# Optimization experiments

Measured on AMD Instinct MI355X. Metric: run time of the kernel, lower is better.

## Reference

```python
import jax, jax.numpy as jnp
import numpy as np

B = 64          # number of scenes/graphs
OBJS = 2048     # objects per scene
N = B * OBJS    # total objects
D = 256         # representation_dim
K = 2           # num_channels


def setup_inputs() -> dict:
    key = jax.random.key(0)
    k1, k2, k3 = jax.random.split(key, 3)
    x_aggregation = jax.random.normal(k1, (N, D), dtype=jnp.float32)
    num_objs = jnp.full((B,), OBJS, dtype=jnp.int32)
    # glorot for att_shared [1, D]: fan_in + fan_out = 1 + D
    std_shared = float(np.sqrt(6.0 / (1 + D)))
    att_shared = jax.random.uniform(k2, (1, D), dtype=jnp.float32,
                                    minval=-std_shared, maxval=std_shared)
    # glorot for att_scale [K, 1]
    std_scale = float(np.sqrt(6.0 / (K + 1)))
    att_scale = jax.random.uniform(k3, (K, 1), dtype=jnp.float32,
                                   minval=-std_scale, maxval=std_scale)
    channel_bias = jnp.zeros((K, D), dtype=jnp.float32)
    return {"x_aggregation": x_aggregation, "num_objs": num_objs,
            "att_shared": att_shared, "att_scale": att_scale,
            "channel_bias": channel_bias}


def reference(x_aggregation, num_objs, att_shared, att_scale, channel_bias):
    batch_idx = jnp.repeat(jnp.arange(B), num_objs, total_repeat_length=N)  # [N]
    # scatter_mean: per-scene context features [B, D]
    seg_sum = jax.ops.segment_sum(x_aggregation, batch_idx, num_segments=B)
    counts = jnp.maximum(num_objs, 1).astype(x_aggregation.dtype)
    ctx = seg_sum / counts[:, None]
    attn_in = jax.nn.leaky_relu(x_aggregation + ctx[batch_idx], negative_slope=0.2)  # [N, D]
    # per-channel logits: ((attn_in + bias[k]) . att_shared) * scale[k]
    base = attn_in @ att_shared[0]                 # [N]
    bias_term = channel_bias @ att_shared[0]       # [K]
    logits = (base[:, None] + bias_term[None, :]) * att_scale[:, 0][None, :]  # [N, K]
    # per-channel segment softmax over objects within each scene
    m = jax.ops.segment_max(logits, batch_idx, num_segments=B)   # [B, K]
    z = jnp.exp(logits - m[batch_idx])
    s = jax.ops.segment_sum(z, batch_idx, num_segments=B)        # [B, K]
    attn_weights = z / s[batch_idx]                              # [N, K]
    # attention-weighted pooling per channel -> [B, D, K]
    weighted = x_aggregation[:, :, None] * attn_weights[:, None, :]  # [N, D, K]
    scene_features = jax.ops.segment_sum(weighted, batch_idx, num_segments=B)
    return scene_features, attn_weights
```

## Files before the change

kernel.cpp:

```cpp
#include <hip/hip_runtime.h>

#define B    64
#define OBJS 2048
#define NTOT (B * OBJS)
#define D    256
#define K    2
#define S1   16
#define CH   (OBJS / S1)
#define RPW  (CH / 4)

#define WS_P1  0
#define WS_UP  (1024 * 256)
#define WS_ZP  (WS_UP + 1024 * 512)
#define WS_E   (WS_ZP + 1024 * 8)
#define WS_CNT (WS_E + NTOT * 2)

static __device__ __forceinline__ float lrelu02(float v) {
    return v > 0.0f ? v : 0.2f * v;
}

__global__ __launch_bounds__(256, 4) void fused_all(
        const float* __restrict__ x,
        const int* __restrict__ num_objs,
        const float* __restrict__ att_scale,
        const float* __restrict__ att_shared,
        const float* __restrict__ channel_bias,
        float* __restrict__ ws,
        float* __restrict__ out) {
    __shared__ float pl[4 * 576];
    __shared__ float esm[4 * 16];
    __shared__ float sctx[D];
    __shared__ float sbt[2];
    __shared__ int   sfin;

    int blk = blockIdx.x;
    int b = blk >> 4;
    int t = threadIdx.x;
    int w = t >> 6, l = t & 63;
    int r = l & 7, sl = l >> 3;
    int row0 = blk * CH + w * RPW;
    int* cntA = (int*)(ws + WS_CNT);
    int* cntF = cntA + B;

    {
        float4 acc = make_float4(0.f, 0.f, 0.f, 0.f);
        const float* px = x + (size_t)row0 * D + 4 * l;
#pragma unroll 8
        for (int j = 0; j < RPW; ++j) {
            float4 v = *(const float4*)(px + (size_t)j * D);
            acc.x += v.x; acc.y += v.y; acc.z += v.z; acc.w += v.w;
        }
        *(float4*)(pl + w * D + 4 * l) = acc;
        __syncthreads();
        if (t < 64) {
            float4 a = ((const float4*)(pl        ))[t];
            float4 e = ((const float4*)(pl +     D))[t];
            float4 f = ((const float4*)(pl + 2 * D))[t];
            float4 g = ((const float4*)(pl + 3 * D))[t];
            float4 s4 = make_float4(a.x + e.x + f.x + g.x, a.y + e.y + f.y + g.y,
                                    a.z + e.z + f.z + g.z, a.w + e.w + f.w + g.w);
            *(float4*)(ws + WS_P1 + blk * D + 4 * t) = s4;
        }
        __syncthreads();
        if (t == 0) {
            __threadfence();
            atomicAdd(&cntA[b], 1);
            while (__hip_atomic_load(&cntA[b], __ATOMIC_RELAXED,
                                     __HIP_MEMORY_SCOPE_AGENT) < S1)
                __builtin_amdgcn_s_sleep(2);
            __threadfence();
        }
        __syncthreads();
    }

    {
        int cnt = num_objs[b]; if (cnt < 1) cnt = 1;
        float inv = 1.0f / (float)cnt;
        float sum = 0.f;
#pragma unroll
        for (int c = 0; c < S1; ++c) sum += ws[WS_P1 + (b * S1 + c) * D + t];
        sctx[t] = sum * inv;
    }
    if (t < 64) {
        float4 a = ((const float4*)att_shared)[t];
#pragma unroll
        for (int k = 0; k < K; ++k) {
            float4 cb = ((const float4*)(channel_bias + k * D))[t];
            float v = a.x * cb.x + a.y * cb.y + a.z * cb.z + a.w * cb.w;
#pragma unroll
            for (int m = 32; m > 0; m >>= 1) v += __shfl_xor(v, m);
            if (t == 0) sbt[k] = v;
        }
    }
    __syncthreads();

    float4 a4   = ((const float4*)att_shared)[l];
    float4 ctx4 = *(const float4*)(sctx + 4 * l);
    float bt0 = sbt[0], bt1 = sbt[1];
    float s0 = att_scale[0], s1 = att_scale[1];

    float4 acc0 = make_float4(0.f, 0.f, 0.f, 0.f);
    float4 acc1 = make_float4(0.f, 0.f, 0.f, 0.f);
    float z0 = 0.f, z1 = 0.f;
    float e0c = 0.f, e1c = 0.f;
    float* pw = pl  + w * 576;
    float* ew = esm + w * 16;
    const float* px = x + (size_t)row0 * D + 4 * l;

#pragma unroll
    for (int g = 0; g < 4; ++g) {
        float4 v0 = *(const float4*)(px + (size_t)(g * 8 + 0) * D);
        float4 v1 = *(const float4*)(px + (size_t)(g * 8 + 1) * D);
        float4 v2 = *(const float4*)(px + (size_t)(g * 8 + 2) * D);
        float4 v3 = *(const float4*)(px + (size_t)(g * 8 + 3) * D);
        float4 v4 = *(const float4*)(px + (size_t)(g * 8 + 4) * D);
        float4 v5 = *(const float4*)(px + (size_t)(g * 8 + 5) * D);
        float4 v6 = *(const float4*)(px + (size_t)(g * 8 + 6) * D);
        float4 v7 = *(const float4*)(px + (size_t)(g * 8 + 7) * D);

#define PDOT(V) (lrelu02((V).x + ctx4.x) * a4.x + lrelu02((V).y + ctx4.y) * a4.y \
               + lrelu02((V).z + ctx4.z) * a4.z + lrelu02((V).w + ctx4.w) * a4.w)
        pw[l * 9 + 0] = PDOT(v0); pw[l * 9 + 1] = PDOT(v1);
        pw[l * 9 + 2] = PDOT(v2); pw[l * 9 + 3] = PDOT(v3);
        pw[l * 9 + 4] = PDOT(v4); pw[l * 9 + 5] = PDOT(v5);
        pw[l * 9 + 6] = PDOT(v6); pw[l * 9 + 7] = PDOT(v7);
#undef PDOT
        float tr = 0.f;
#pragma unroll
        for (int q = 0; q < 8; ++q) tr += pw[(sl * 8 + q) * 9 + r];
        tr += __shfl_xor(tr, 8);
        tr += __shfl_xor(tr, 16);
        tr += __shfl_xor(tr, 32);

        float e0 = __expf((tr + bt0) * s0);
        float e1 = __expf((tr + bt1) * s1);
        if (((l >> 3) & 3) == g) { e0c = e0; e1c = e1; }
        if (l < 8) { ew[2 * l] = e0; ew[2 * l + 1] = e1; }
        float4 E0 = *(const float4*)(ew + 0);
        float4 E1 = *(const float4*)(ew + 4);
        float4 E2 = *(const float4*)(ew + 8);
        float4 E3 = *(const float4*)(ew + 12);
        z0 += E0.x + E0.z + E1.x + E1.z + E2.x + E2.z + E3.x + E3.z;
        z1 += E0.y + E0.w + E1.y + E1.w + E2.y + E2.w + E3.y + E3.w;

#define ACC(V, EA, EB) { acc0.x += (V).x * (EA); acc0.y += (V).y * (EA);      \
                         acc0.z += (V).z * (EA); acc0.w += (V).w * (EA);      \
                         acc1.x += (V).x * (EB); acc1.y += (V).y * (EB);      \
                         acc1.z += (V).z * (EB); acc1.w += (V).w * (EB); }
        ACC(v0, E0.x, E0.y) ACC(v1, E0.z, E0.w)
        ACC(v2, E1.x, E1.y) ACC(v3, E1.z, E1.w)
        ACC(v4, E2.x, E2.y) ACC(v5, E2.z, E2.w)
        ACC(v6, E3.x, E3.y) ACC(v7, E3.z, E3.w)
#undef ACC
    }

    if (l < 32) ((float2*)(ws + WS_E))[row0 + l] = make_float2(e0c, e1c);
    if (l == 0) {
        ws[WS_ZP + blk * 8 + w * 2 + 0] = z0;
        ws[WS_ZP + blk * 8 + w * 2 + 1] = z1;
    }
    __syncthreads();
    {
        int base = w * (D * K) + l * 8;
        pl[base + 0] = acc0.x; pl[base + 1] = acc1.x;
        pl[base + 2] = acc0.y; pl[base + 3] = acc1.y;
        pl[base + 4] = acc0.z; pl[base + 5] = acc1.z;
        pl[base + 6] = acc0.w; pl[base + 7] = acc1.w;
    }
    __syncthreads();
    if (t < 128) {
        float4 a = ((const float4*)(pl       ))[t];
        float4 e = ((const float4*)(pl +  512))[t];
        float4 f = ((const float4*)(pl + 1024))[t];
        float4 g = ((const float4*)(pl + 1536))[t];
        float4 s4 = make_float4(a.x + e.x + f.x + g.x, a.y + e.y + f.y + g.y,
                                a.z + e.z + f.z + g.z, a.w + e.w + f.w + g.w);
        *(float4*)(ws + WS_UP + (size_t)blk * (D * K) + 4 * t) = s4;
    }

    __syncthreads();
    if (t == 0) {
        __threadfence();
        int old = atomicAdd(&cntF[b], 1);
        sfin = (old == S1 - 1) ? 1 : 0;
        if (sfin) __threadfence();
    }
    __syncthreads();
    if (!sfin) return;

    if (w < 2) {
        float v = ws[WS_ZP + (b * S1 + (l >> 2)) * 8 + (l & 3) * 2 + w];
#pragma unroll
        for (int m = 32; m > 0; m >>= 1) v += __shfl_xor(v, m);
        if (l == 0) sbt[w] = v;
    }
    __syncthreads();
    float zf0 = sbt[0], zf1 = sbt[1];
    float iz0 = 1.0f / zf0, iz1 = 1.0f / zf1;

#pragma unroll
    for (int j = t; j < D * K; j += 256) {
        float ssum = 0.f;
#pragma unroll
        for (int c = 0; c < S1; ++c) ssum += ws[WS_UP + (b * S1 + c) * (D * K) + j];
        out[b * (D * K) + j] = ssum * ((j & 1) ? iz1 : iz0);
    }
    const float4* E = (const float4*)(ws + WS_E);
    float4* W = (float4*)(out + B * D * K);
#pragma unroll
    for (int i = t; i < OBJS / 2; i += 256) {
        float4 e4 = E[b * (OBJS / 2) + i];
        W[b * (OBJS / 2) + i] = make_float4(e4.x * iz0, e4.y * iz1, e4.z * iz0, e4.w * iz1);
    }
}

__global__ __launch_bounds__(256) void k1_partial(const float* __restrict__ x,
                                                  float* __restrict__ ws) {
    __shared__ float red[4 * D];
    int blk = blockIdx.x;
    int w = threadIdx.x >> 6, l = threadIdx.x & 63;
    int row0 = blk * CH + w * RPW;

    float4 acc = make_float4(0.f, 0.f, 0.f, 0.f);
    const float* px = x + (size_t)row0 * D + 4 * l;
#pragma unroll 8
    for (int j = 0; j < RPW; ++j) {
        float4 v = *(const float4*)(px + (size_t)j * D);
        acc.x += v.x; acc.y += v.y; acc.z += v.z; acc.w += v.w;
    }
    *(float4*)(red + w * D + 4 * l) = acc;
    __syncthreads();
    int t = threadIdx.x;
    if (t < 64) {
        float4 a = ((const float4*)(red        ))[t];
        float4 e = ((const float4*)(red +     D))[t];
        float4 f = ((const float4*)(red + 2 * D))[t];
        float4 g = ((const float4*)(red + 3 * D))[t];
        float4 s = make_float4(a.x + e.x + f.x + g.x, a.y + e.y + f.y + g.y,
                               a.z + e.z + f.z + g.z, a.w + e.w + f.w + g.w);
        *(float4*)(ws + WS_P1 + blk * D + 4 * t) = s;
    }
}

__global__ __launch_bounds__(256) void k2_main(const float* __restrict__ x,
                                               const int* __restrict__ num_objs,
                                               const float* __restrict__ att_scale,
                                               const float* __restrict__ att_shared,
                                               const float* __restrict__ channel_bias,
                                               float* __restrict__ ws) {
    __shared__ float pl[4 * 576];
    __shared__ float esm[4 * 16];
    __shared__ float sctx[D];
    __shared__ float sbt[2];

    int blk = blockIdx.x;
    int b = blk >> 4;
    int t = threadIdx.x;
    int w = t >> 6, l = t & 63;
    int r = l & 7, s = l >> 3;
    int row0 = blk * CH + w * RPW;

    {
        int cnt = num_objs[b]; if (cnt < 1) cnt = 1;
        float inv = 1.0f / (float)cnt;
        float sum = 0.f;
#pragma unroll
        for (int c = 0; c < S1; ++c) sum += ws[WS_P1 + (b * S1 + c) * D + t];
        sctx[t] = sum * inv;
    }
    if (t < 64) {
        float4 a = ((const float4*)att_shared)[t];
#pragma unroll
        for (int k = 0; k < K; ++k) {
            float4 cb = ((const float4*)(channel_bias + k * D))[t];
            float v = a.x * cb.x + a.y * cb.y + a.z * cb.z + a.w * cb.w;
#pragma unroll
            for (int m = 32; m > 0; m >>= 1) v += __shfl_xor(v, m);
            if (t == 0) sbt[k] = v;
        }
    }
    __syncthreads();

    float4 a4   = ((const float4*)att_shared)[l];
    float4 ctx4 = *(const float4*)(sctx + 4 * l);
    float bt0 = sbt[0], bt1 = sbt[1];
    float s0 = att_scale[0], s1 = att_scale[1];

    float4 acc0 = make_float4(0.f, 0.f, 0.f, 0.f);
    float4 acc1 = make_float4(0.f, 0.f, 0.f, 0.f);
    float z0 = 0.f, z1 = 0.f;
    float e0c = 0.f, e1c = 0.f;
    float* pw = pl  + w * 576;
    float* ew = esm + w * 16;
    const float* px = x + (size_t)row0 * D + 4 * l;

#pragma unroll
    for (int g = 0; g < 4; ++g) {
        float4 v0 = *(const float4*)(px + (size_t)(g * 8 + 0) * D);
        float4 v1 = *(const float4*)(px + (size_t)(g * 8 + 1) * D);
        float4 v2 = *(const float4*)(px + (size_t)(g * 8 + 2) * D);
        float4 v3 = *(const float4*)(px + (size_t)(g * 8 + 3) * D);
        float4 v4 = *(const float4*)(px + (size_t)(g * 8 + 4) * D);
        float4 v5 = *(const float4*)(px + (size_t)(g * 8 + 5) * D);
        float4 v6 = *(const float4*)(px + (size_t)(g * 8 + 6) * D);
        float4 v7 = *(const float4*)(px + (size_t)(g * 8 + 7) * D);

#define PDOT(V) (lrelu02((V).x + ctx4.x) * a4.x + lrelu02((V).y + ctx4.y) * a4.y \
               + lrelu02((V).z + ctx4.z) * a4.z + lrelu02((V).w + ctx4.w) * a4.w)
        pw[l * 9 + 0] = PDOT(v0); pw[l * 9 + 1] = PDOT(v1);
        pw[l * 9 + 2] = PDOT(v2); pw[l * 9 + 3] = PDOT(v3);
        pw[l * 9 + 4] = PDOT(v4); pw[l * 9 + 5] = PDOT(v5);
        pw[l * 9 + 6] = PDOT(v6); pw[l * 9 + 7] = PDOT(v7);
#undef PDOT
        float tr = 0.f;
#pragma unroll
        for (int q = 0; q < 8; ++q) tr += pw[(s * 8 + q) * 9 + r];
        tr += __shfl_xor(tr, 8);
        tr += __shfl_xor(tr, 16);
        tr += __shfl_xor(tr, 32);

        float e0 = __expf((tr + bt0) * s0);
        float e1 = __expf((tr + bt1) * s1);
        if (((l >> 3) & 3) == g) { e0c = e0; e1c = e1; }
        if (l < 8) { ew[2 * l] = e0; ew[2 * l + 1] = e1; }
        float4 E0 = *(const float4*)(ew + 0);
        float4 E1 = *(const float4*)(ew + 4);
        float4 E2 = *(const float4*)(ew + 8);
        float4 E3 = *(const float4*)(ew + 12);
        z0 += E0.x + E0.z + E1.x + E1.z + E2.x + E2.z + E3.x + E3.z;
        z1 += E0.y + E0.w + E1.y + E1.w + E2.y + E2.w + E3.y + E3.w;

#define ACC(V, EA, EB) { acc0.x += (V).x * (EA); acc0.y += (V).y * (EA);      \
                         acc0.z += (V).z * (EA); acc0.w += (V).w * (EA);      \
                         acc1.x += (V).x * (EB); acc1.y += (V).y * (EB);      \
                         acc1.z += (V).z * (EB); acc1.w += (V).w * (EB); }
        ACC(v0, E0.x, E0.y) ACC(v1, E0.z, E0.w)
        ACC(v2, E1.x, E1.y) ACC(v3, E1.z, E1.w)
        ACC(v4, E2.x, E2.y) ACC(v5, E2.z, E2.w)
        ACC(v6, E3.x, E3.y) ACC(v7, E3.z, E3.w)
#undef ACC
    }

    if (l < 32) ((float2*)(ws + WS_E))[row0 + l] = make_float2(e0c, e1c);
    if (l == 0) {
        ws[WS_ZP + blk * 8 + w * 2 + 0] = z0;
        ws[WS_ZP + blk * 8 + w * 2 + 1] = z1;
    }
    __syncthreads();
    {
        int base = w * (D * K) + l * 8;
        pl[base + 0] = acc0.x; pl[base + 1] = acc1.x;
        pl[base + 2] = acc0.y; pl[base + 3] = acc1.y;
        pl[base + 4] = acc0.z; pl[base + 5] = acc1.z;
        pl[base + 6] = acc0.w; pl[base + 7] = acc1.w;
    }
    __syncthreads();
    if (t < 128) {
        float4 a = ((const float4*)(pl       ))[t];
        float4 e = ((const float4*)(pl +  512))[t];
        float4 f = ((const float4*)(pl + 1024))[t];
        float4 g = ((const float4*)(pl + 1536))[t];
        float4 s4 = make_float4(a.x + e.x + f.x + g.x, a.y + e.y + f.y + g.y,
                                a.z + e.z + f.z + g.z, a.w + e.w + f.w + g.w);
        *(float4*)(ws + WS_UP + (size_t)blk * (D * K) + 4 * t) = s4;
    }
}

__global__ __launch_bounds__(256) void k3_final(const float* __restrict__ ws,
                                                float* __restrict__ out) {
    __shared__ float zsh[2];
    int b = blockIdx.x;
    int t = threadIdx.x;
    int w = t >> 6, l = t & 63;

    if (w < 2) {
        float v = ws[WS_ZP + (b * S1 + (l >> 2)) * 8 + (l & 3) * 2 + w];
#pragma unroll
        for (int m = 32; m > 0; m >>= 1) v += __shfl_xor(v, m);
        if (l == 0) zsh[w] = v;
    }
    __syncthreads();
    float z0 = zsh[0], z1 = zsh[1];
    float iz0 = 1.0f / z0, iz1 = 1.0f / z1;

#pragma unroll
    for (int j = t; j < D * K; j += 256) {
        float s = 0.f;
#pragma unroll
        for (int c = 0; c < S1; ++c) s += ws[WS_UP + (b * S1 + c) * (D * K) + j];
        out[b * (D * K) + j] = s * ((j & 1) ? iz1 : iz0);
    }
    const float4* E = (const float4*)(ws + WS_E);
    float4* W = (float4*)(out + B * D * K);
#pragma unroll
    for (int i = t; i < OBJS / 2; i += 256) {
        float4 e = E[b * (OBJS / 2) + i];
        W[b * (OBJS / 2) + i] = make_float4(e.x * iz0, e.y * iz1, e.z * iz0, e.w * iz1);
    }
}

extern "C" void kernel_launch(void* const* d_in, const int* in_sizes, int n_in,
                              void* d_out, int out_size, void* d_ws, size_t ws_size,
                              hipStream_t stream) {
    const float* x            = (const float*)d_in[0];
    const int*   num_objs     = (const int*)d_in[1];
    const float* att_shared   = (const float*)d_in[2];
    const float* att_scale    = (const float*)d_in[3];
    const float* channel_bias = (const float*)d_in[4];
    float* ws  = (float*)d_ws;
    float* out = (float*)d_out;

    static int coop_ok = -1;
    if (coop_ok < 0) {
        int nb = 0;
        hipError_t e = hipOccupancyMaxActiveBlocksPerMultiprocessor(
                &nb, fused_all, 256, 0);
        coop_ok = (e == hipSuccess && nb >= 4) ? 1 : 0;
    }

    if (coop_ok) {
        hipMemsetAsync((char*)d_ws + sizeof(float) * (size_t)WS_CNT, 0,
                       2 * B * sizeof(int), stream);
        void* args[] = {(void*)&x, (void*)&num_objs, (void*)&att_scale,
                        (void*)&att_shared, (void*)&channel_bias,
                        (void*)&ws, (void*)&out};
        hipError_t e = hipLaunchCooperativeKernel((void*)fused_all,
                                                  dim3(B * S1), dim3(256),
                                                  args, 0, stream);
        if (e == hipSuccess) return;
        coop_ok = 0;
    }

    k1_partial<<<B * S1, 256, 0, stream>>>(x, ws);
    k2_main<<<B * S1, 256, 0, stream>>>(x, num_objs, att_scale, att_shared,
                                        channel_bias, ws);
    k3_final<<<B, 256, 0, stream>>>(ws, out);
}
```

Measured before the change: 222.3 us.

## Cache x rows in registers and LDS to avoid second global read

The cooperative fused kernel now runs 256 blocks (4 per scene, one per CU) instead of 1024. Each wave keeps its first 80 rows in registers (kp) and the next 32 rows in 128 KB of dynamic LDS while computing the context sum. The softmax/pooling pass then reuses those buffered rows and reloads only the last 16 rows from global memory, which removes most of the second read of x. In exchange, occupancy drops to one large block per CU with very high register pressure, which risks spills and leaves little latency hiding.

Result: no change. 221.1 us (-0.5%).

```diff
diff --git a/kernel.cpp b/kernel.cpp
--- a/kernel.cpp
+++ b/kernel.cpp
@@ -5,6 +5,12 @@
 #define NTOT (B * OBJS)
 #define D    256
 #define K    2
+
+#define NBLK 256
+#define BPS  4
+#define CHF  (OBJS / BPS)
+#define RPWF (CHF / 4)
+
 #define S1   16
 #define CH   (OBJS / S1)
 #define RPW  (CH / 4)
@@ -19,7 +25,7 @@
     return v > 0.0f ? v : 0.2f * v;
 }
 
-__global__ __launch_bounds__(256, 4) void fused_all(
+__global__ __launch_bounds__(256, 1) void fused_all(
         const float* __restrict__ x,
         const int* __restrict__ num_objs,
         const float* __restrict__ att_scale,
@@ -27,6 +33,7 @@
         const float* __restrict__ channel_bias,
         float* __restrict__ ws,
         float* __restrict__ out) {
+    extern __shared__ float4 xbuf4[];
     __shared__ float pl[4 * 576];
     __shared__ float esm[4 * 16];
     __shared__ float sctx[D];
@@ -34,44 +41,277 @@
     __shared__ int   sfin;
 
     int blk = blockIdx.x;
+    int b = blk / BPS;
+    int t = threadIdx.x;
+    int w = t >> 6, l = t & 63;
+    int r = l & 7, sl = l >> 3;
+    int row0 = blk * CHF + w * RPWF;
+    int* cntA = (int*)(ws + WS_CNT);
+    int* cntF = cntA + B;
+
+    float4 kp[10][8];
+    float4* xw = xbuf4 + (size_t)w * (32 * 64);
+    const float* px = x + (size_t)row0 * D + 4 * l;
+
+    float4 acc = make_float4(0.f, 0.f, 0.f, 0.f);
+#pragma unroll
+    for (int g = 0; g < 10; ++g) {
+#pragma unroll
+        for (int j = 0; j < 8; ++j) {
+            float4 v = *(const float4*)(px + (size_t)(g * 8 + j) * D);
+            kp[g][j] = v;
+            acc.x += v.x; acc.y += v.y; acc.z += v.z; acc.w += v.w;
+        }
+    }
+#pragma unroll
+    for (int gl = 0; gl < 32; ++gl) {
+        float4 v = *(const float4*)(px + (size_t)(80 + gl) * D);
+        xw[gl * 64 + l] = v;
+        acc.x += v.x; acc.y += v.y; acc.z += v.z; acc.w += v.w;
+    }
+#pragma unroll
+    for (int j = 0; j < 16; ++j) {
+        float4 v = *(const float4*)(px + (size_t)(112 + j) * D);
+        acc.x += v.x; acc.y += v.y; acc.z += v.z; acc.w += v.w;
+    }
+    *(float4*)(pl + w * D + 4 * l) = acc;
+    __syncthreads();
+    if (t < 64) {
+        float4 a = ((const float4*)(pl        ))[t];
+        float4 e = ((const float4*)(pl +     D))[t];
+        float4 f = ((const float4*)(pl + 2 * D))[t];
+        float4 g = ((const float4*)(pl + 3 * D))[t];
+        float4 s4 = make_float4(a.x + e.x + f.x + g.x, a.y + e.y + f.y + g.y,
+                                a.z + e.z + f.z + g.z, a.w + e.w + f.w + g.w);
+        *(float4*)(ws + WS_P1 + blk * D + 4 * t) = s4;
+    }
+    __syncthreads();
+    if (t == 0) {
+        __threadfence();
+        atomicAdd(&cntA[b], 1);
+        while (__hip_atomic_load(&cntA[b], __ATOMIC_RELAXED,
+                                 __HIP_MEMORY_SCOPE_AGENT) < BPS)
+            __builtin_amdgcn_s_sleep(2);
+        __threadfence();
+    }
+    __syncthreads();
+
+    {
+        int cnt = num_objs[b]; if (cnt < 1) cnt = 1;
+        float inv = 1.0f / (float)cnt;
+        float sum = 0.f;
+#pragma unroll
+        for (int c = 0; c < BPS; ++c) sum += ws[WS_P1 + (b * BPS + c) * D + t];
+        sctx[t] = sum * inv;
+    }
+    if (t < 64) {
+        float4 a = ((const float4*)att_shared)[t];
+#pragma unroll
+        for (int k = 0; k < K; ++k) {
+            float4 cb = ((const float4*)(channel_bias + k * D))[t];
+            float v = a.x * cb.x + a.y * cb.y + a.z * cb.z + a.w * cb.w;
+#pragma unroll
+            for (int m = 32; m > 0; m >>= 1) v += __shfl_xor(v, m);
+            if (t == 0) sbt[k] = v;
+        }
+    }
+    __syncthreads();
+
+    float4 a4   = ((const float4*)att_shared)[l];
+    float4 ctx4 = *(const float4*)(sctx + 4 * l);
+    float bt0 = sbt[0], bt1 = sbt[1];
+    float s0 = att_scale[0], s1 = att_scale[1];
+
+    float4 acc0 = make_float4(0.f, 0.f, 0.f, 0.f);
+    float4 acc1 = make_float4(0.f, 0.f, 0.f, 0.f);
+    float z0 = 0.f, z1 = 0.f;
+    float e0c = 0.f, e1c = 0.f;
+    float e0d = 0.f, e1d = 0.f;
+    float* pw = pl  + w * 576;
+    float* ew = esm + w * 16;
+
+#define PD(V) (lrelu02((V).x + ctx4.x) * a4.x + lrelu02((V).y + ctx4.y) * a4.y \
+             + lrelu02((V).z + ctx4.z) * a4.z + lrelu02((V).w + ctx4.w) * a4.w)
+#define ACC(V, EA, EB) { acc0.x += (V).x * (EA); acc0.y += (V).y * (EA);      \
+                         acc0.z += (V).z * (EA); acc0.w += (V).w * (EA);      \
+                         acc1.x += (V).x * (EB); acc1.y += (V).y * (EB);      \
+                         acc1.z += (V).z * (EB); acc1.w += (V).w * (EB); }
+#define PROC_GROUP(GI, L0, L1, L2, L3, L4, L5, L6, L7) {                      \
+    pw[l * 9 + 0] = PD(L0); pw[l * 9 + 1] = PD(L1);                           \
+    pw[l * 9 + 2] = PD(L2); pw[l * 9 + 3] = PD(L3);                           \
+    pw[l * 9 + 4] = PD(L4); pw[l * 9 + 5] = PD(L5);                           \
+    pw[l * 9 + 6] = PD(L6); pw[l * 9 + 7] = PD(L7);                           \
+    float tr = 0.f;                                                           \
+    _Pragma("unroll")                                                         \
+    for (int q = 0; q < 8; ++q) tr += pw[(sl * 8 + q) * 9 + r];               \
+    tr += __shfl_xor(tr, 8);                                                  \
+    tr += __shfl_xor(tr, 16);                                                 \
+    tr += __shfl_xor(tr, 32);                                                 \
+    float e0 = __expf((tr + bt0) * s0);                                       \
+    float e1 = __expf((tr + bt1) * s1);                                       \
+    if ((GI) == (l >> 3))     { e0c = e0; e1c = e1; }                         \
+    if ((GI) == 8 + (l >> 3)) { e0d = e0; e1d = e1; }                         \
+    if (l < 8) { ew[2 * l] = e0; ew[2 * l + 1] = e1; }                        \
+    float4 E0 = *(const float4*)(ew + 0);                                     \
+    float4 E1 = *(const float4*)(ew + 4);                                     \
+    float4 E2 = *(const float4*)(ew + 8);                                     \
+    float4 E3 = *(const float4*)(ew + 12);                                    \
+    z0 += E0.x + E0.z + E1.x + E1.z + E2.x + E2.z + E3.x + E3.z;              \
+    z1 += E0.y + E0.w + E1.y + E1.w + E2.y + E2.w + E3.y + E3.w;              \
+    ACC(L0, E0.x, E0.y) ACC(L1, E0.z, E0.w)                                   \
+    ACC(L2, E1.x, E1.y) ACC(L3, E1.z, E1.w)                                   \
+    ACC(L4, E2.x, E2.y) ACC(L5, E2.z, E2.w)                                   \
+    ACC(L6, E3.x, E3.y) ACC(L7, E3.z, E3.w)                                   \
+}
+#define PG_KP(G) PROC_GROUP(G, kp[G][0], kp[G][1], kp[G][2], kp[G][3],        \
+                               kp[G][4], kp[G][5], kp[G][6], kp[G][7])
+
+    PG_KP(0) PG_KP(1) PG_KP(2) PG_KP(3)
+    float4 sa[8], sb[8];
+#pragma unroll
+    for (int j = 0; j < 8; ++j) sa[j] = *(const float4*)(px + (size_t)(112 + j) * D);
+#pragma unroll
+    for (int j = 0; j < 8; ++j) sb[j] = *(const float4*)(px + (size_t)(120 + j) * D);
+
+    PG_KP(4) PG_KP(5) PG_KP(6) PG_KP(7) PG_KP(8) PG_KP(9)
+    {
+        float4 q0 = xw[0 * 64 + l], q1 = xw[1 * 64 + l], q2 = xw[2 * 64 + l],
+               q3 = xw[3 * 64 + l], q4 = xw[4 * 64 + l], q5 = xw[5 * 64 + l],
+               q6 = xw[6 * 64 + l], q7 = xw[7 * 64 + l];
+        PROC_GROUP(10, q0, q1, q2, q3, q4, q5, q6, q7)
+    }
+    {
+        float4 q0 = xw[8 * 64 + l], q1 = xw[9 * 64 + l], q2 = xw[10 * 64 + l],
+               q3 = xw[11 * 64 + l], q4 = xw[12 * 64 + l], q5 = xw[13 * 64 + l],
+               q6 = xw[14 * 64 + l], q7 = xw[15 * 64 + l];
+        PROC_GROUP(11, q0, q1, q2, q3, q4, q5, q6, q7)
+    }
+    {
+        float4 q0 = xw[16 * 64 + l], q1 = xw[17 * 64 + l], q2 = xw[18 * 64 + l],
+               q3 = xw[19 * 64 + l], q4 = xw[20 * 64 + l], q5 = xw[21 * 64 + l],
+               q6 = xw[22 * 64 + l], q7 = xw[23 * 64 + l];
+        PROC_GROUP(12, q0, q1, q2, q3, q4, q5, q6, q7)
+    }
+    {
+        float4 q0 = xw[24 * 64 + l], q1 = xw[25 * 64 + l], q2 = xw[26 * 64 + l],
+               q3 = xw[27 * 64 + l], q4 = xw[28 * 64 + l], q5 = xw[29 * 64 + l],
+               q6 = xw[30 * 64 + l], q7 = xw[31 * 64 + l];
+        PROC_GROUP(13, q0, q1, q2, q3, q4, q5, q6, q7)
+    }
+    PROC_GROUP(14, sa[0], sa[1], sa[2], sa[3], sa[4], sa[5], sa[6], sa[7])
+    PROC_GROUP(15, sb[0], sb[1], sb[2], sb[3], sb[4], sb[5], sb[6], sb[7])
+#undef PG_KP
+#undef PROC_GROUP
+#undef ACC
+#undef PD
+
+    ((float2*)(ws + WS_E))[row0 + l]      = make_float2(e0c, e1c);
+    ((float2*)(ws + WS_E))[row0 + 64 + l] = make_float2(e0d, e1d);
+    if (l == 0) {
+        ws[WS_ZP + blk * 8 + w * 2 + 0] = z0;
+        ws[WS_ZP + blk * 8 + w * 2 + 1] = z1;
+    }
+    __syncthreads();
+    {
+        int base = w * (D * K) + l * 8;
+        pl[base + 0] = acc0.x; pl[base + 1] = acc1.x;
+        pl[base + 2] = acc0.y; pl[base + 3] = acc1.y;
+        pl[base + 4] = acc0.z; pl[base + 5] = acc1.z;
+        pl[base + 6] = acc0.w; pl[base + 7] = acc1.w;
+    }
+    __syncthreads();
+    if (t < 128) {
+        float4 a = ((const float4*)(pl       ))[t];
+        float4 e = ((const float4*)(pl +  512))[t];
+        float4 f = ((const float4*)(pl + 1024))[t];
+        float4 g = ((const float4*)(pl + 1536))[t];
+        float4 s4 = make_float4(a.x + e.x + f.x + g.x, a.y + e.y + f.y + g.y,
+                                a.z + e.z + f.z + g.z, a.w + e.w + f.w + g.w);
+        *(float4*)(ws + WS_UP + (size_t)blk * (D * K) + 4 * t) = s4;
+    }
+
+    __syncthreads();
+    if (t == 0) {
+        __threadfence();
+        int old = atomicAdd(&cntF[b], 1);
+        sfin = (old == BPS - 1) ? 1 : 0;
+        if (sfin) __threadfence();
+    }
+    __syncthreads();
+    if (!sfin) return;
+
+    if (w < 2) {
+        float v = (l < 16)
+                ? ws[WS_ZP + (b * BPS + (l >> 2)) * 8 + (l & 3) * 2 + w] : 0.f;
+        v += __shfl_xor(v, 1); v += __shfl_xor(v, 2);
+        v += __shfl_xor(v, 4); v += __shfl_xor(v, 8);
+        if (l == 0) sbt[w] = v;
+    }
+    __syncthreads();
+    float zf0 = sbt[0], zf1 = sbt[1];
+    float iz0 = 1.0f / zf0, iz1 = 1.0f / zf1;
+
+#pragma unroll
+    for (int j = t; j < D * K; j += 256) {
+        float ssum = 0.f;
+#pragma unroll
+        for (int c = 0; c < BPS; ++c) ssum += ws[WS_UP + (b * BPS + c) * (D * K) + j];
+        out[b * (D * K) + j] = ssum * ((j & 1) ? iz1 : iz0);
+    }
+    const float4* E = (const float4*)(ws + WS_E);
+    float4* W = (float4*)(out + B * D * K);
+#pragma unroll
+    for (int i = t; i < OBJS / 2; i += 256) {
+        float4 e4 = E[b * (OBJS / 2) + i];
+        W[b * (OBJS / 2) + i] = make_float4(e4.x * iz0, e4.y * iz1, e4.z * iz0, e4.w * iz1);
+    }
+}
+
+__global__ __launch_bounds__(256) void k1_partial(const float* __restrict__ x,
+                                                  float* __restrict__ ws) {
+    __shared__ float red[4 * D];
+    int blk = blockIdx.x;
+    int w = threadIdx.x >> 6, l = threadIdx.x & 63;
+    int row0 = blk * CH + w * RPW;
+
+    float4 acc = make_float4(0.f, 0.f, 0.f, 0.f);
+    const float* px = x + (size_t)row0 * D + 4 * l;
+#pragma unroll 8
+    for (int j = 0; j < RPW; ++j) {
+        float4 v = *(const float4*)(px + (size_t)j * D);
+        acc.x += v.x; acc.y += v.y; acc.z += v.z; acc.w += v.w;
+    }
+    *(float4*)(red + w * D + 4 * l) = acc;
+    __syncthreads();
+    int t = threadIdx.x;
+    if (t < 64) {
+        float4 a = ((const float4*)(red        ))[t];
+        float4 e = ((const float4*)(red +     D))[t];
+        float4 f = ((const float4*)(red + 2 * D))[t];
+        float4 g = ((const float4*)(red + 3 * D))[t];
+        float4 s = make_float4(a.x + e.x + f.x + g.x, a.y + e.y + f.y + g.y,
+                               a.z + e.z + f.z + g.z, a.w + e.w + f.w + g.w);
+        *(float4*)(ws + WS_P1 + blk * D + 4 * t) = s;
+    }
+}
+
+__global__ __launch_bounds__(256) void k2_main(const float* __restrict__ x,
+                                               const int* __restrict__ num_objs,
+                                               const float* __restrict__ att_scale,
+                                               const float* __restrict__ att_shared,
+                                               const float* __restrict__ channel_bias,
+                                               float* __restrict__ ws) {
+    __shared__ float pl[4 * 576];
+    __shared__ float esm[4 * 16];
+    __shared__ float sctx[D];
+    __shared__ float sbt[2];
+
+    int blk = blockIdx.x;
     int b = blk >> 4;
     int t = threadIdx.x;
     int w = t >> 6, l = t & 63;
-    int r = l & 7, sl = l >> 3;
+    int r = l & 7, s = l >> 3;
     int row0 = blk * CH + w * RPW;
-    int* cntA = (int*)(ws + WS_CNT);
-    int* cntF = cntA + B;
-
-    {
-        float4 acc = make_float4(0.f, 0.f, 0.f, 0.f);
-        const float* px = x + (size_t)row0 * D + 4 * l;
-#pragma unroll 8
-        for (int j = 0; j < RPW; ++j) {
-            float4 v = *(const float4*)(px + (size_t)j * D);
-            acc.x += v.x; acc.y += v.y; acc.z += v.z; acc.w += v.w;
-        }
-        *(float4*)(pl + w * D + 4 * l) = acc;
-        __syncthreads();
-        if (t < 64) {
-            float4 a = ((const float4*)(pl        ))[t];
-            float4 e = ((const float4*)(pl +     D))[t];
-            float4 f = ((const float4*)(pl + 2 * D))[t];
-            float4 g = ((const float4*)(pl + 3 * D))[t];
-            float4 s4 = make_float4(a.x + e.x + f.x + g.x, a.y + e.y + f.y + g.y,
-                                    a.z + e.z + f.z + g.z, a.w + e.w + f.w + g.w);
-            *(float4*)(ws + WS_P1 + blk * D + 4 * t) = s4;
-        }
-        __syncthreads();
-        if (t == 0) {
-            __threadfence();
-            atomicAdd(&cntA[b], 1);
-            while (__hip_atomic_load(&cntA[b], __ATOMIC_RELAXED,
-                                     __HIP_MEMORY_SCOPE_AGENT) < S1)
-                __builtin_amdgcn_s_sleep(2);
-            __threadfence();
-        }
-        __syncthreads();
-    }
 
     {
         int cnt = num_objs[b]; if (cnt < 1) cnt = 1;
@@ -127,7 +367,7 @@
 #undef PDOT
         float tr = 0.f;
 #pragma unroll
-        for (int q = 0; q < 8; ++q) tr += pw[(sl * 8 + q) * 9 + r];
+        for (int q = 0; q < 8; ++q) tr += pw[(s * 8 + q) * 9 + r];
         tr += __shfl_xor(tr, 8);
         tr += __shfl_xor(tr, 16);
         tr += __shfl_xor(tr, 32);
@@ -177,193 +417,6 @@
                                 a.z + e.z + f.z + g.z, a.w + e.w + f.w + g.w);
         *(float4*)(ws + WS_UP + (size_t)blk * (D * K) + 4 * t) = s4;
     }
-
-    __syncthreads();
-    if (t == 0) {
-        __threadfence();
-        int old = atomicAdd(&cntF[b], 1);
-        sfin = (old == S1 - 1) ? 1 : 0;
-        if (sfin) __threadfence();
-    }
-    __syncthreads();
-    if (!sfin) return;
-
-    if (w < 2) {
-        float v = ws[WS_ZP + (b * S1 + (l >> 2)) * 8 + (l & 3) * 2 + w];
-#pragma unroll
-        for (int m = 32; m > 0; m >>= 1) v += __shfl_xor(v, m);
-        if (l == 0) sbt[w] = v;
-    }
-    __syncthreads();
-    float zf0 = sbt[0], zf1 = sbt[1];
-    float iz0 = 1.0f / zf0, iz1 = 1.0f / zf1;
-
-#pragma unroll
-    for (int j = t; j < D * K; j += 256) {
-        float ssum = 0.f;
-#pragma unroll
-        for (int c = 0; c < S1; ++c) ssum += ws[WS_UP + (b * S1 + c) * (D * K) + j];
-        out[b * (D * K) + j] = ssum * ((j & 1) ? iz1 : iz0);
-    }
-    const float4* E = (const float4*)(ws + WS_E);
-    float4* W = (float4*)(out + B * D * K);
-#pragma unroll
-    for (int i = t; i < OBJS / 2; i += 256) {
-        float4 e4 = E[b * (OBJS / 2) + i];
-        W[b * (OBJS / 2) + i] = make_float4(e4.x * iz0, e4.y * iz1, e4.z * iz0, e4.w * iz1);
-    }
-}
-
-__global__ __launch_bounds__(256) void k1_partial(const float* __restrict__ x,
-                                                  float* __restrict__ ws) {
-    __shared__ float red[4 * D];
-    int blk = blockIdx.x;
-    int w = threadIdx.x >> 6, l = threadIdx.x & 63;
-    int row0 = blk * CH + w * RPW;
-
-    float4 acc = make_float4(0.f, 0.f, 0.f, 0.f);
-    const float* px = x + (size_t)row0 * D + 4 * l;
-#pragma unroll 8
-    for (int j = 0; j < RPW; ++j) {
-        float4 v = *(const float4*)(px + (size_t)j * D);
-        acc.x += v.x; acc.y += v.y; acc.z += v.z; acc.w += v.w;
-    }
-    *(float4*)(red + w * D + 4 * l) = acc;
-    __syncthreads();
-    int t = threadIdx.x;
-    if (t < 64) {
-        float4 a = ((const float4*)(red        ))[t];
-        float4 e = ((const float4*)(red +     D))[t];
-        float4 f = ((const float4*)(red + 2 * D))[t];
-        float4 g = ((const float4*)(red + 3 * D))[t];
-        float4 s = make_float4(a.x + e.x + f.x + g.x, a.y + e.y + f.y + g.y,
-                               a.z + e.z + f.z + g.z, a.w + e.w + f.w + g.w);
-        *(float4*)(ws + WS_P1 + blk * D + 4 * t) = s;
-    }
-}
-
-__global__ __launch_bounds__(256) void k2_main(const float* __restrict__ x,
-                                               const int* __restrict__ num_objs,
-                                               const float* __restrict__ att_scale,
-                                               const float* __restrict__ att_shared,
-                                               const float* __restrict__ channel_bias,
-                                               float* __restrict__ ws) {
-    __shared__ float pl[4 * 576];
-    __shared__ float esm[4 * 16];
-    __shared__ float sctx[D];
-    __shared__ float sbt[2];
-
-    int blk = blockIdx.x;
-    int b = blk >> 4;
-    int t = threadIdx.x;
-    int w = t >> 6, l = t & 63;
-    int r = l & 7, s = l >> 3;
-    int row0 = blk * CH + w * RPW;
-
-    {
-        int cnt = num_objs[b]; if (cnt < 1) cnt = 1;
-        float inv = 1.0f / (float)cnt;
-        float sum = 0.f;
-#pragma unroll
-        for (int c = 0; c < S1; ++c) sum += ws[WS_P1 + (b * S1 + c) * D + t];
-        sctx[t] = sum * inv;
-    }
-    if (t < 64) {
-        float4 a = ((const float4*)att_shared)[t];
-#pragma unroll
-        for (int k = 0; k < K; ++k) {
-            float4 cb = ((const float4*)(channel_bias + k * D))[t];
-            float v = a.x * cb.x + a.y * cb.y + a.z * cb.z + a.w * cb.w;
-#pragma unroll
-            for (int m = 32; m > 0; m >>= 1) v += __shfl_xor(v, m);
-            if (t == 0) sbt[k] = v;
-        }
-    }
-    __syncthreads();
-
-    float4 a4   = ((const float4*)att_shared)[l];
-    float4 ctx4 = *(const float4*)(sctx + 4 * l);
-    float bt0 = sbt[0], bt1 = sbt[1];
-    float s0 = att_scale[0], s1 = att_scale[1];
-
-    float4 acc0 = make_float4(0.f, 0.f, 0.f, 0.f);
-    float4 acc1 = make_float4(0.f, 0.f, 0.f, 0.f);
-    float z0 = 0.f, z1 = 0.f;
-    float e0c = 0.f, e1c = 0.f;
-    float* pw = pl  + w * 576;
-    float* ew = esm + w * 16;
-    const float* px = x + (size_t)row0 * D + 4 * l;
-
-#pragma unroll
-    for (int g = 0; g < 4; ++g) {
-        float4 v0 = *(const float4*)(px + (size_t)(g * 8 + 0) * D);
-        float4 v1 = *(const float4*)(px + (size_t)(g * 8 + 1) * D);
-        float4 v2 = *(const float4*)(px + (size_t)(g * 8 + 2) * D);
-        float4 v3 = *(const float4*)(px + (size_t)(g * 8 + 3) * D);
-        float4 v4 = *(const float4*)(px + (size_t)(g * 8 + 4) * D);
-        float4 v5 = *(const float4*)(px + (size_t)(g * 8 + 5) * D);
-        float4 v6 = *(const float4*)(px + (size_t)(g * 8 + 6) * D);
-        float4 v7 = *(const float4*)(px + (size_t)(g * 8 + 7) * D);
-
-#define PDOT(V) (lrelu02((V).x + ctx4.x) * a4.x + lrelu02((V).y + ctx4.y) * a4.y \
-               + lrelu02((V).z + ctx4.z) * a4.z + lrelu02((V).w + ctx4.w) * a4.w)
-        pw[l * 9 + 0] = PDOT(v0); pw[l * 9 + 1] = PDOT(v1);
-        pw[l * 9 + 2] = PDOT(v2); pw[l * 9 + 3] = PDOT(v3);
-        pw[l * 9 + 4] = PDOT(v4); pw[l * 9 + 5] = PDOT(v5);
-        pw[l * 9 + 6] = PDOT(v6); pw[l * 9 + 7] = PDOT(v7);
-#undef PDOT
-        float tr = 0.f;
-#pragma unroll
-        for (int q = 0; q < 8; ++q) tr += pw[(s * 8 + q) * 9 + r];
-        tr += __shfl_xor(tr, 8);
-        tr += __shfl_xor(tr, 16);
-        tr += __shfl_xor(tr, 32);
-
-        float e0 = __expf((tr + bt0) * s0);
-        float e1 = __expf((tr + bt1) * s1);
-        if (((l >> 3) & 3) == g) { e0c = e0; e1c = e1; }
-        if (l < 8) { ew[2 * l] = e0; ew[2 * l + 1] = e1; }
-        float4 E0 = *(const float4*)(ew + 0);
-        float4 E1 = *(const float4*)(ew + 4);
-        float4 E2 = *(const float4*)(ew + 8);
-        float4 E3 = *(const float4*)(ew + 12);
-        z0 += E0.x + E0.z + E1.x + E1.z + E2.x + E2.z + E3.x + E3.z;
-        z1 += E0.y + E0.w + E1.y + E1.w + E2.y + E2.w + E3.y + E3.w;
-
-#define ACC(V, EA, EB) { acc0.x += (V).x * (EA); acc0.y += (V).y * (EA);      \
-                         acc0.z += (V).z * (EA); acc0.w += (V).w * (EA);      \
-                         acc1.x += (V).x * (EB); acc1.y += (V).y * (EB);      \
-                         acc1.z += (V).z * (EB); acc1.w += (V).w * (EB); }
-        ACC(v0, E0.x, E0.y) ACC(v1, E0.z, E0.w)
-        ACC(v2, E1.x, E1.y) ACC(v3, E1.z, E1.w)
-        ACC(v4, E2.x, E2.y) ACC(v5, E2.z, E2.w)
-        ACC(v6, E3.x, E3.y) ACC(v7, E3.z, E3.w)
-#undef ACC
-    }
-
-    if (l < 32) ((float2*)(ws + WS_E))[row0 + l] = make_float2(e0c, e1c);
-    if (l == 0) {
-        ws[WS_ZP + blk * 8 + w * 2 + 0] = z0;
-        ws[WS_ZP + blk * 8 + w * 2 + 1] = z1;
-    }
-    __syncthreads();
-    {
-        int base = w * (D * K) + l * 8;
-        pl[base + 0] = acc0.x; pl[base + 1] = acc1.x;
-        pl[base + 2] = acc0.y; pl[base + 3] = acc1.y;
-        pl[base + 4] = acc0.z; pl[base + 5] = acc1.z;
-        pl[base + 6] = acc0.w; pl[base + 7] = acc1.w;
-    }
-    __syncthreads();
-    if (t < 128) {
-        float4 a = ((const float4*)(pl       ))[t];
-        float4 e = ((const float4*)(pl +  512))[t];
-        float4 f = ((const float4*)(pl + 1024))[t];
-        float4 g = ((const float4*)(pl + 1536))[t];
-        float4 s4 = make_float4(a.x + e.x + f.x + g.x, a.y + e.y + f.y + g.y,
-                                a.z + e.z + f.z + g.z, a.w + e.w + f.w + g.w);
-        *(float4*)(ws + WS_UP + (size_t)blk * (D * K) + 4 * t) = s4;
-    }
 }
 
 __global__ __launch_bounds__(256) void k3_final(const float* __restrict__ ws,
@@ -410,12 +463,17 @@
     float* ws  = (float*)d_ws;
     float* out = (float*)d_out;
 
+    const int DYN_LDS = 4 * 32 * 64 * (int)sizeof(float4);
+
     static int coop_ok = -1;
     if (coop_ok < 0) {
+        (void)hipFuncSetAttribute((const void*)fused_all,
+                                  hipFuncAttributeMaxDynamicSharedMemorySize,
+                                  DYN_LDS);
         int nb = 0;
         hipError_t e = hipOccupancyMaxActiveBlocksPerMultiprocessor(
-                &nb, fused_all, 256, 0);
-        coop_ok = (e == hipSuccess && nb >= 4) ? 1 : 0;
+                &nb, fused_all, 256, DYN_LDS);
+        coop_ok = (e == hipSuccess && nb >= 1) ? 1 : 0;
     }
 
     if (coop_ok) {
@@ -425,8 +483,8 @@
                         (void*)&att_shared, (void*)&channel_bias,
                         (void*)&ws, (void*)&out};
         hipError_t e = hipLaunchCooperativeKernel((void*)fused_all,
-                                                  dim3(B * S1), dim3(256),
-                                                  args, 0, stream);
+                                                  dim3(NBLK), dim3(256),
+                                                  args, DYN_LDS, stream);
         if (e == hipSuccess) return;
         coop_ok = 0;
     }
```
